# Optimization experiments

Measured on AMD Instinct MI355X. Metric: run time of the kernel, lower is better.

The kernel has to match this reference:

```python
import jax, jax.numpy as jnp
import numpy as np

N = 100000   # nodes
E = 1600000  # edges
IN = 128     # in_dim
H = 64       # hidden_dim
EPS = 1e-5


def layer_norm(x, g, b):
    mu = x.mean(-1, keepdims=True)
    v = ((x - mu) ** 2).mean(-1, keepdims=True)
    return (x - mu) * jax.lax.rsqrt(v + EPS) * g + b


def gcn_conv(x, W, b, src, dst, dinv):
    # PyG GCNConv: x' = D^{-1/2}(A+I)D^{-1/2} X W + b (degrees include self-loops)
    h = x @ W                                   # [N, H]
    coef = dinv[src] * dinv[dst]                # [E]
    agg = jax.ops.segment_sum(h[src] * coef[:, None], dst, num_segments=N)
    agg = agg + h * (dinv * dinv)[:, None]      # self-loop term
    return agg + b


def setup_inputs() -> dict:
    key = jax.random.key(0)
    ks = jax.random.split(key, 12)
    inp = {
        "x": jax.random.normal(ks[0], (N, IN), jnp.float32),
        "edge_index": jax.random.randint(ks[1], (2, E), 0, N, dtype=jnp.int64
                                         if jax.config.jax_enable_x64 else jnp.int32),
    }
    dims = [(IN, H), (H, H), (H, H)]
    for i, (di, do) in enumerate(dims, start=1):
        inp[f"W{i}"] = jax.random.normal(ks[2 * i], (di, do), jnp.float32) / np.sqrt(di)
        inp[f"b{i}"] = jnp.zeros((do,), jnp.float32)
        inp[f"g{i}"] = jnp.ones((do,), jnp.float32)
        inp[f"be{i}"] = jnp.zeros((do,), jnp.float32)
    inp["Wh"] = jax.random.normal(ks[11], (H, 1), jnp.float32) / np.sqrt(H)
    inp["bh"] = jnp.zeros((1,), jnp.float32)
    return inp


def reference(x, edge_index, W1, b1, g1, be1, W2, b2, g2, be2, W3, b3, g3, be3, Wh, bh):
    src, dst = edge_index[0], edge_index[1]
    deg = jax.ops.segment_sum(jnp.ones((E,), x.dtype), dst, num_segments=N) + 1.0
    dinv = jax.lax.rsqrt(deg)
    for W, b, g, be in ((W1, b1, g1, be1), (W2, b2, g2, be2), (W3, b3, g3, be3)):
        x = gcn_conv(x, W, b, src, dst, dinv)
        x = layer_norm(x, g, be)
        x = jax.nn.gelu(x, approximate=False)  # F.gelu default = exact erf
        # dropout omitted (eval mode / deterministic reference)
    return (x @ Wh + bh).squeeze(-1)  # [N]
```

## Files before the change

### kernel.cpp

```cpp
#include <hip/hip_runtime.h>
#include <math.h>

#define NODES 100000
#define EDGES 1600000
#define NBUCK 196
#define BCAP2 12288
#define EPB 4096
#define BINB 391
#define GEMMB 1563

typedef __attribute__((ext_vector_type(8))) short short8;
typedef __attribute__((ext_vector_type(4))) float floatx4;
typedef __attribute__((ext_vector_type(4))) unsigned uv4;

__device__ __forceinline__ float gsum8(float x) {
#pragma unroll
  for (int o = 4; o > 0; o >>= 1) x += __shfl_xor(x, o, 64);
  return x;
}

__device__ __forceinline__ short f2bf(float f) {
  union { float f; unsigned u; } v;
  v.f = f;
  unsigned r = 0x7fffu + ((v.u >> 16) & 1u);
  return (short)((v.u + r) >> 16);
}
__device__ __forceinline__ float bflo(unsigned p) {
  union { unsigned u; float f; } v; v.u = p << 16; return v.f;
}
__device__ __forceinline__ float bfhi(unsigned p) {
  union { unsigned u; float f; } v; v.u = p & 0xffff0000u; return v.f;
}

#define BIN_SMEM (4 * 256 * 4 + EPB * 4 + EPB)
__device__ __forceinline__ void bin_body(char* smemraw, int b, const int* __restrict__ src,
                                         const int* __restrict__ dst, int* __restrict__ bins,
                                         int* __restrict__ gcur) {
  int* cnt = (int*)smemraw;
  int* gb = cnt + 256;
  int* lb = gb + 256;
  int* lcur = lb + 256;
  int* rec = lcur + 256;
  unsigned char* rbk = (unsigned char*)(rec + EPB);
  int t = threadIdx.x;
  cnt[t] = 0;
  __syncthreads();
  int base = b * EPB;
  int nv = EDGES - base; if (nv > EPB) nv = EPB;
  int s[16], d[16];
#pragma unroll
  for (int j = 0; j < 16; ++j) {
    int e = base + j * 256 + t;
    if (e < EDGES) {
      s[j] = src[e];
      d[j] = dst[e];
      atomicAdd(&cnt[d[j] >> 9], 1);
    } else {
      d[j] = -1;
    }
  }
  __syncthreads();
  int c = cnt[t];
  lb[t] = c;
  __syncthreads();
  for (int o = 1; o < 256; o <<= 1) {
    int u = (t >= o) ? lb[t - o] : 0;
    __syncthreads();
    lb[t] += u;
    __syncthreads();
  }
  int ex = lb[t] - c;
  gb[t] = (c > 0) ? atomicAdd(&gcur[t], c) : 0;
  __syncthreads();
  lb[t] = ex;
  lcur[t] = ex;
  __syncthreads();
#pragma unroll
  for (int j = 0; j < 16; ++j) {
    if (d[j] >= 0) {
      int bk = d[j] >> 9;
      int lp = atomicAdd(&lcur[bk], 1);
      rec[lp] = s[j] | ((d[j] & 511) << 17);
      rbk[lp] = (unsigned char)bk;
    }
  }
  __syncthreads();
  for (int i = t; i < nv; i += 256) {
    int bk = rbk[i];
    int pos = gb[bk] + (i - lb[bk]);
    if (pos < BCAP2) bins[bk * BCAP2 + pos] = rec[i];
  }
}

#define FILL_SMEM (256 * 4 + 512 * 4 + 512 * 4 + 4 * 4 + BCAP2 * 4)
__device__ __forceinline__ void fill_body(char* smemraw, int b, const int* __restrict__ bins,
                                          const int* __restrict__ gcur, int* __restrict__ rowptr,
                                          float* __restrict__ dinv, int* __restrict__ csr) {
  int* bsm = (int*)smemraw;
  int* cnt = bsm + 256;
  int* cur = cnt + 512;
  int* wtot = cur + 512;
  int* stage = wtot + 4;
  int t = threadIdx.x;
  int v = 0;
  if (t < NBUCK) { v = gcur[t]; if (v > BCAP2) v = BCAP2; }
  bsm[t] = v;
  cnt[t] = 0; cnt[t + 256] = 0;
  __syncthreads();
  for (int o = 1; o < 256; o <<= 1) {
    int u = (t >= o) ? bsm[t - o] : 0;
    __syncthreads();
    bsm[t] += u;
    __syncthreads();
  }
  if (b == 0 && t == NBUCK - 1) rowptr[NODES] = bsm[t];
  int cb = gcur[b]; if (cb > BCAP2) cb = BCAP2;
  int bbase = bsm[b] - cb;
  const int* bp = &bins[(size_t)b * BCAP2];
  for (int i = t; i < cb; i += 256)
    atomicAdd(&cnt[(bp[i] >> 17) & 511], 1);
  __syncthreads();
  int a0 = cnt[2 * t], a1 = cnt[2 * t + 1];
  int sum2 = a0 + a1;
  int lane = t & 63, w = t >> 6;
  int inc = sum2;
#pragma unroll
  for (int o = 1; o < 64; o <<= 1) {
    int u = __shfl_up(inc, o, 64);
    if (lane >= o) inc += u;
  }
  if (lane == 63) wtot[w] = inc;
  __syncthreads();
  int wpre = 0;
  for (int ww = 0; ww < w; ++ww) wpre += wtot[ww];
  int l0 = wpre + inc - sum2;
  int l1 = l0 + a0;
  int n0 = b * 512 + 2 * t, n1 = n0 + 1;
  if (n0 < NODES) { rowptr[n0] = bbase + l0; dinv[n0] = rsqrtf((float)a0 + 1.0f); }
  if (n1 < NODES) { rowptr[n1] = bbase + l1; dinv[n1] = rsqrtf((float)a1 + 1.0f); }
  cur[2 * t] = l0; cur[2 * t + 1] = l1;
  __syncthreads();
  for (int i = t; i < cb; i += 256) {
    int pk = bp[i];
    int lp = atomicAdd(&cur[(pk >> 17) & 511], 1);
    stage[lp] = pk & 0x1FFFF;
  }
  __syncthreads();
  for (int i = t; i < cb; i += 256) csr[bbase + i] = stage[i];
}

#define GEMM_SMEM (64 * 136 * 2)
__device__ __forceinline__ void gemm_body(char* smemraw, int tile0, const float* __restrict__ x,
                                          const float* __restrict__ W, short* __restrict__ hs) {
  constexpr int K = 128, KP = K + 8;
  short* wt = (short*)smemraw;
  for (int idx = threadIdx.x; idx < K * 64; idx += 256) {
    int k = idx >> 6, n = idx & 63;
    wt[n * KP + k] = f2bf(W[idx]);
  }
  __syncthreads();
  int wid = threadIdx.x >> 6, lane = threadIdx.x & 63;
  int tile = tile0 + wid;
  if (tile * 16 >= NODES) return;
  int m = lane & 15, q = lane >> 4;

  short8 bfr[4][K / 32];
#pragma unroll
  for (int ct = 0; ct < 4; ++ct)
#pragma unroll
    for (int ks = 0; ks < K / 32; ++ks)
      bfr[ct][ks] = *reinterpret_cast<const short8*>(&wt[(ct * 16 + m) * KP + ks * 32 + q * 8]);

  floatx4 acc[4];
#pragma unroll
  for (int ct = 0; ct < 4; ++ct) acc[ct] = {0.f, 0.f, 0.f, 0.f};
  int r0 = tile * 16;
#pragma unroll
  for (int ks = 0; ks < K / 32; ++ks) {
    const float* xp = &x[(size_t)(r0 + m) * K + ks * 32 + q * 8];
    floatx4 a0 = *reinterpret_cast<const floatx4*>(xp);
    floatx4 a1 = *reinterpret_cast<const floatx4*>(xp + 4);
    short8 af;
#pragma unroll
    for (int j = 0; j < 4; ++j) { af[j] = f2bf(a0[j]); af[4 + j] = f2bf(a1[j]); }
#pragma unroll
    for (int ct = 0; ct < 4; ++ct)
      acc[ct] = __builtin_amdgcn_mfma_f32_16x16x32_bf16(af, bfr[ct][ks], acc[ct], 0, 0, 0);
  }
#pragma unroll
  for (int ct = 0; ct < 4; ++ct)
#pragma unroll
    for (int r = 0; r < 4; ++r) {
      int row = r0 + q * 4 + r, col = ct * 16 + m;
      hs[row * 64 + col] = f2bf(acc[ct][r]);
    }
}

__device__ __forceinline__ void prepw_body(int p, const float* __restrict__ W2,
                                           const float* __restrict__ W3,
                                           short* __restrict__ wt2, short* __restrict__ wt3) {
  const float* W = (p < 4) ? W2 : W3;
  short* wt = (p < 4) ? wt2 : wt3;
  int b0 = (p & 3) * 1024;
  for (int i = threadIdx.x; i < 1024; i += 256) {
    int e = b0 + i;
    int k = e >> 6, n = e & 63;
    wt[n * 72 + k] = f2bf(W[e]);
  }
}

template <bool PRESCALED>
__device__ __forceinline__ void do_agg(const uv4* __restrict__ hsv, const float* __restrict__ dinv,
                                       const int* __restrict__ csr, int n, int e0, int e1,
                                       int lane, float dn, float acc[8]) {
  int q = lane & 7, srcb = lane & 0x38;
  uv4 sv = hsv[(size_t)n * 8 + q];
#pragma unroll
  for (int w = 0; w < 4; ++w) {
    float lo = bflo(sv[w]), hi = bfhi(sv[w]);
    if constexpr (PRESCALED) { acc[2 * w] = lo; acc[2 * w + 1] = hi; }
    else { acc[2 * w] = lo * dn; acc[2 * w + 1] = hi * dn; }
  }
  for (int base = e0; base < e1; base += 8) {
    int cnt = e1 - base;
    if (cnt > 8) cnt = 8;
    int a = base + (q < cnt ? q : 0);
    int sidx = csr[a];
    float gq = 1.0f;
    if constexpr (!PRESCALED) gq = dinv[sidx];
    int s[8]; float wj[8];
#pragma unroll
    for (int j = 0; j < 8; ++j) {
      s[j] = __shfl(sidx, srcb | j, 64);
      if constexpr (!PRESCALED) {
        float bj = __shfl(gq, srcb | j, 64);
        wj[j] = (j < cnt) ? bj : 0.0f;
      } else {
        wj[j] = 1.0f;
      }
    }
    uv4 v[8];
#pragma unroll
    for (int j = 0; j < 8; ++j) v[j] = hsv[(size_t)s[j] * 8 + q];
    if constexpr (PRESCALED) {
      if (cnt == 8) {
#pragma unroll
        for (int j = 0; j < 8; ++j)
#pragma unroll
          for (int w = 0; w < 4; ++w) { acc[2 * w] += bflo(v[j][w]); acc[2 * w + 1] += bfhi(v[j][w]); }
      } else {
#pragma unroll
        for (int j = 0; j < 8; ++j)
          if (j < cnt)
#pragma unroll
            for (int w = 0; w < 4; ++w) { acc[2 * w] += bflo(v[j][w]); acc[2 * w + 1] += bfhi(v[j][w]); }
      }
    } else {
#pragma unroll
      for (int j = 0; j < 8; ++j)
#pragma unroll
        for (int w = 0; w < 4; ++w) {
          acc[2 * w]     += wj[j] * bflo(v[j][w]);
          acc[2 * w + 1] += wj[j] * bfhi(v[j][w]);
        }
    }
  }
}

template <bool PRESCALED>
__global__ __launch_bounds__(256) void k_aggg(const short* __restrict__ hs,
                                              const float* __restrict__ dinv,
                                              const int* __restrict__ rowptr,
                                              const int* __restrict__ csr,
                                              const float* __restrict__ bias,
                                              const float* __restrict__ gam,
                                              const float* __restrict__ bet,
                                              const short* __restrict__ wtg,
                                              short* __restrict__ hsn) {
  __shared__ __align__(16) short wt[64 * 72];
  __shared__ __align__(16) short ut[32 * 72];
  int t = threadIdx.x;
  {
    const int* wp = (const int*)wtg;
    int* wd = (int*)wt;
    for (int idx = t; idx < 2304; idx += 256) wd[idx] = wp[idx];
  }
  const uv4* hsv = (const uv4*)hs;
  int lane = t & 63, wid = t >> 6;
  int g = lane >> 3, q = lane & 7;
  int nb0 = blockIdx.x * 32;
  int r = wid * 8 + g;
  int n = nb0 + r;
  int e0 = rowptr[n], e1 = rowptr[n + 1];
  float dn = dinv[n];
  float acc[8];
  do_agg<PRESCALED>(hsv, dinv, csr, n, e0, e1, lane, dn, acc);

  const floatx4* bi4 = (const floatx4*)bias;
  floatx4 b0 = bi4[q * 2], b1 = bi4[q * 2 + 1];
#pragma unroll
  for (int f = 0; f < 4; ++f) { acc[f] = acc[f] * dn + b0[f]; acc[f + 4] = acc[f + 4] * dn + b1[f]; }

  float lsum = 0.f;
#pragma unroll
  for (int f = 0; f < 8; ++f) lsum += acc[f];
  float mu = gsum8(lsum) * (1.0f / 64.0f);
  float d[8], lvar = 0.f;
#pragma unroll
  for (int f = 0; f < 8; ++f) { d[f] = acc[f] - mu; lvar += d[f] * d[f]; }
  float rs = rsqrtf(gsum8(lvar) * (1.0f / 64.0f) + 1e-5f);
  const floatx4* gm4 = (const floatx4*)gam;
  const floatx4* bt4 = (const floatx4*)bet;
  floatx4 g0 = gm4[q * 2], g1 = gm4[q * 2 + 1];
  floatx4 t0 = bt4[q * 2], t1 = bt4[q * 2 + 1];
  short8 us;
#pragma unroll
  for (int f = 0; f < 8; ++f) {
    float gv = (f < 4) ? g0[f] : g1[f - 4];
    float tv = (f < 4) ? t0[f] : t1[f - 4];
    float vv = d[f] * rs * gv + tv;
    float u = 0.5f * vv * (1.0f + erff(vv * 0.70710678118654752f));
    us[f] = f2bf(u * dn);
  }
  *reinterpret_cast<short8*>(&ut[r * 72 + q * 8]) = us;
  __syncthreads();

  int m = lane & 15, q2 = lane >> 4;
  int tile = wid >> 1, cb = (wid & 1) * 2;
  short8 bfr[2][2];
#pragma unroll
  for (int ct = 0; ct < 2; ++ct)
#pragma unroll
    for (int ks = 0; ks < 2; ++ks)
      bfr[ct][ks] = *reinterpret_cast<const short8*>(&wt[((cb + ct) * 16 + m) * 72 + ks * 32 + q2 * 8]);
  floatx4 ac[2];
#pragma unroll
  for (int ct = 0; ct < 2; ++ct) ac[ct] = {0.f, 0.f, 0.f, 0.f};
#pragma unroll
  for (int ks = 0; ks < 2; ++ks) {
    short8 af = *reinterpret_cast<const short8*>(&ut[(tile * 16 + m) * 72 + ks * 32 + q2 * 8]);
#pragma unroll
    for (int ct = 0; ct < 2; ++ct)
      ac[ct] = __builtin_amdgcn_mfma_f32_16x16x32_bf16(af, bfr[ct][ks], ac[ct], 0, 0, 0);
  }
#pragma unroll
  for (int ct = 0; ct < 2; ++ct)
#pragma unroll
    for (int rr = 0; rr < 4; ++rr) {
      int row = nb0 + tile * 16 + q2 * 4 + rr, col = (cb + ct) * 16 + m;
      hsn[row * 64 + col] = f2bf(ac[ct][rr]);
    }
}

__global__ __launch_bounds__(256) void k_agg_fin(const short* __restrict__ hs,
                                                 const float* __restrict__ dinv,
                                                 const int* __restrict__ rowptr,
                                                 const int* __restrict__ csr,
                                                 const float* __restrict__ bias,
                                                 const float* __restrict__ gam,
                                                 const float* __restrict__ bet,
                                                 const float* __restrict__ Wh,
                                                 const float* __restrict__ bh,
                                                 float* __restrict__ out) {
  const uv4* hsv = (const uv4*)hs;
  int lane = threadIdx.x & 63, wid = threadIdx.x >> 6;
  int g = lane >> 3, q = lane & 7;
  int n = blockIdx.x * 32 + wid * 8 + g;
  int e0 = rowptr[n], e1 = rowptr[n + 1];
  float dn = dinv[n];
  float acc[8];
  do_agg<true>(hsv, dinv, csr, n, e0, e1, lane, dn, acc);
  const floatx4* bi4 = (const floatx4*)bias;
  floatx4 b0 = bi4[q * 2], b1 = bi4[q * 2 + 1];
#pragma unroll
  for (int f = 0; f < 4; ++f) { acc[f] = acc[f] * dn + b0[f]; acc[f + 4] = acc[f + 4] * dn + b1[f]; }
  float lsum = 0.f;
#pragma unroll
  for (int f = 0; f < 8; ++f) lsum += acc[f];
  float mu = gsum8(lsum) * (1.0f / 64.0f);
  float d[8], lvar = 0.f;
#pragma unroll
  for (int f = 0; f < 8; ++f) { d[f] = acc[f] - mu; lvar += d[f] * d[f]; }
  float rs = rsqrtf(gsum8(lvar) * (1.0f / 64.0f) + 1e-5f);
  const floatx4* gm4 = (const floatx4*)gam;
  const floatx4* bt4 = (const floatx4*)bet;
  floatx4 g0 = gm4[q * 2], g1 = gm4[q * 2 + 1];
  floatx4 t0 = bt4[q * 2], t1 = bt4[q * 2 + 1];
  const floatx4* wh4 = (const floatx4*)Wh;
  floatx4 w0 = wh4[q * 2], w1 = wh4[q * 2 + 1];
  float lp = 0.f;
#pragma unroll
  for (int f = 0; f < 8; ++f) {
    float gv = (f < 4) ? g0[f] : g1[f - 4];
    float tv = (f < 4) ? t0[f] : t1[f - 4];
    float wv = (f < 4) ? w0[f] : w1[f - 4];
    float vv = d[f] * rs * gv + tv;
    float u = 0.5f * vv * (1.0f + erff(vv * 0.70710678118654752f));
    lp += u * wv;
  }
  float p = gsum8(lp);
  if (q == 0) out[n] = p + bh[0];
}

__global__ __launch_bounds__(256) void k_pre1(const int* __restrict__ src, const int* __restrict__ dst,
                                              int* __restrict__ bins, int* __restrict__ gcur,
                                              const float* __restrict__ x, const float* __restrict__ W1,
                                              short* __restrict__ hs,
                                              const float* __restrict__ W2, const float* __restrict__ W3,
                                              short* __restrict__ wt2, short* __restrict__ wt3) {
  __shared__ __align__(16) char smem[BIN_SMEM];
  int b = blockIdx.x;
  if (b < BINB) bin_body(smem, b, src, dst, bins, gcur);
  else if (b < BINB + GEMMB) gemm_body(smem, (b - BINB) * 4, x, W1, hs);
  else prepw_body(b - BINB - GEMMB, W2, W3, wt2, wt3);
}

__global__ __launch_bounds__(256) void k_pre2(const int* __restrict__ bins, const int* __restrict__ gcur,
                                              int* __restrict__ rowptr, float* __restrict__ dinv,
                                              int* __restrict__ csr) {
  __shared__ __align__(16) char smem[FILL_SMEM];
  fill_body(smem, blockIdx.x, bins, gcur, rowptr, dinv, csr);
}

__global__ __launch_bounds__(256) void k_bin2(const int* src, const int* dst, int* bins, int* gcur) {
  __shared__ __align__(16) char smem[BIN_SMEM];
  bin_body(smem, blockIdx.x, src, dst, bins, gcur);
}
__global__ __launch_bounds__(256) void k_fillb2(const int* bins, const int* gcur, int* rowptr,
                                                float* dinv, int* csr) {
  __shared__ __align__(16) char smem[FILL_SMEM];
  fill_body(smem, blockIdx.x, bins, gcur, rowptr, dinv, csr);
}
__global__ __launch_bounds__(256) void k_gemm(const float* x, const float* W, short* hs) {
  __shared__ __align__(16) char smem[GEMM_SMEM];
  gemm_body(smem, blockIdx.x * 4, x, W, hs);
}
__global__ __launch_bounds__(256) void k_prepw(const float* W2, const float* W3, short* wt2, short* wt3) {
  prepw_body(blockIdx.x, W2, W3, wt2, wt3);
}

extern "C" void kernel_launch(void* const* d_in, const int* in_sizes, int n_in,
                              void* d_out, int out_size, void* d_ws, size_t ws_size,
                              hipStream_t stream) {
  const float* x  = (const float*)d_in[0];
  const int* ei   = (const int*)d_in[1];
  const float* W1 = (const float*)d_in[2];
  const float* b1 = (const float*)d_in[3];
  const float* g1 = (const float*)d_in[4];
  const float* be1= (const float*)d_in[5];
  const float* W2 = (const float*)d_in[6];
  const float* b2 = (const float*)d_in[7];
  const float* g2 = (const float*)d_in[8];
  const float* be2= (const float*)d_in[9];
  const float* W3 = (const float*)d_in[10];
  const float* b3 = (const float*)d_in[11];
  const float* g3 = (const float*)d_in[12];
  const float* be3= (const float*)d_in[13];
  const float* Wh = (const float*)d_in[14];
  const float* bh = (const float*)d_in[15];
  const int* srcp = ei;
  const int* dstp = ei + EDGES;

  char* ws = (char*)d_ws;
  size_t off = 0;
  auto take = [&](size_t bytes) {
    char* p = ws + off;
    off = (off + bytes + 255) & ~(size_t)255;
    return p;
  };
  float* dinv = (float*)take((size_t)NODES * 4);
  int* rowptr = (int*)take((size_t)(NODES + 1) * 4);
  int* csr    = (int*)take((size_t)EDGES * 4);
  short* hs_a = (short*)take((size_t)NODES * 64 * 2);
  short* hs_b = (short*)take((size_t)NODES * 64 * 2);
  short* wt2  = (short*)take((size_t)64 * 72 * 2);
  short* wt3  = (short*)take((size_t)64 * 72 * 2);

  size_t bins_sz = (size_t)NBUCK * BCAP2 * 4;
  bool overlap = (ws_size >= off + bins_sz + 4096);
  int* bins; int* gcur;
  if (overlap) {
    bins = (int*)take(bins_sz);
    gcur = (int*)take((size_t)NBUCK * 4);
  } else {
    bins = (int*)hs_a;
    gcur = (int*)hs_b;
  }

  (void)hipMemsetAsync(gcur, 0, (size_t)NBUCK * 4, stream);
  if (overlap) {
    k_pre1<<<BINB + GEMMB + 8, 256, 0, stream>>>(srcp, dstp, bins, gcur, x, W1, hs_a, W2, W3, wt2, wt3);
    k_pre2<<<NBUCK, 256, 0, stream>>>(bins, gcur, rowptr, dinv, csr);
  } else {
    k_bin2<<<BINB, 256, 0, stream>>>(srcp, dstp, bins, gcur);
    k_fillb2<<<NBUCK, 256, 0, stream>>>(bins, gcur, rowptr, dinv, csr);
    k_gemm<<<GEMMB, 256, 0, stream>>>(x, W1, hs_a);
    k_prepw<<<8, 256, 0, stream>>>(W2, W3, wt2, wt3);
  }
  k_aggg<false><<<NODES / 32, 256, 0, stream>>>(hs_a, dinv, rowptr, csr, b1, g1, be1, wt2, hs_b);
  k_aggg<true><<<NODES / 32, 256, 0, stream>>>(hs_b, dinv, rowptr, csr, b2, g2, be2, wt3, hs_a);
  k_agg_fin<<<NODES / 32, 256, 0, stream>>>(hs_a, dinv, rowptr, csr, b3, g3, be3, Wh, bh, (float*)d_out);
}
```

Measured before the change: 270.3 us.

## Prescale layer-1 features in fill pass and widen gather batches to 24 edges

The CSR fill kernel now multiplies the first-layer bf16 features by each node's dinv in place, so every aggregation layer can use the same prescaled gather path. That removes the per-edge dinv lookups and multiplies from layer 1. The gather loop now issues 24 neighbor loads per batch instead of 8, behind a scheduling barrier, to keep more memory requests in flight. Launch bounds are set to one block per SM minimum. The extra bf16 rounding of the prescaled features adds small numerical error, and the larger register footprint may lower occupancy.

```diff
diff --git a/kernel.cpp b/kernel.cpp
--- a/kernel.cpp
+++ b/kernel.cpp
@@ -30,6 +30,12 @@
 }
 __device__ __forceinline__ float bfhi(unsigned p) {
   union { unsigned u; float f; } v; v.u = p & 0xffff0000u; return v.f;
+}
+__device__ __forceinline__ unsigned scale2(unsigned p, float s) {
+  float lo = bflo(p) * s, hi = bfhi(p) * s;
+  unsigned ulo = (unsigned)(unsigned short)f2bf(lo);
+  unsigned uhi = (unsigned)(unsigned short)f2bf(hi);
+  return ulo | (uhi << 16);
 }
 
 #define BIN_SMEM (4 * 256 * 4 + EPB * 4 + EPB)
@@ -92,15 +98,17 @@
   }
 }
 
-#define FILL_SMEM (256 * 4 + 512 * 4 + 512 * 4 + 4 * 4 + BCAP2 * 4)
+#define FILL_SMEM (256 * 4 + 512 * 4 + 512 * 4 + 4 * 4 + BCAP2 * 4 + 512 * 4)
 __device__ __forceinline__ void fill_body(char* smemraw, int b, const int* __restrict__ bins,
                                           const int* __restrict__ gcur, int* __restrict__ rowptr,
-                                          float* __restrict__ dinv, int* __restrict__ csr) {
+                                          float* __restrict__ dinv, int* __restrict__ csr,
+                                          short* __restrict__ hs) {
   int* bsm = (int*)smemraw;
   int* cnt = bsm + 256;
   int* cur = cnt + 512;
   int* wtot = cur + 512;
   int* stage = wtot + 4;
+  float* dinvs = (float*)(stage + BCAP2);
   int t = threadIdx.x;
   int v = 0;
   if (t < NBUCK) { v = gcur[t]; if (v > BCAP2) v = BCAP2; }
@@ -136,8 +144,10 @@
   int l0 = wpre + inc - sum2;
   int l1 = l0 + a0;
   int n0 = b * 512 + 2 * t, n1 = n0 + 1;
-  if (n0 < NODES) { rowptr[n0] = bbase + l0; dinv[n0] = rsqrtf((float)a0 + 1.0f); }
-  if (n1 < NODES) { rowptr[n1] = bbase + l1; dinv[n1] = rsqrtf((float)a1 + 1.0f); }
+  float dv0 = rsqrtf((float)a0 + 1.0f), dv1 = rsqrtf((float)a1 + 1.0f);
+  if (n0 < NODES) { rowptr[n0] = bbase + l0; dinv[n0] = dv0; }
+  if (n1 < NODES) { rowptr[n1] = bbase + l1; dinv[n1] = dv1; }
+  dinvs[2 * t] = dv0; dinvs[2 * t + 1] = dv1;
   cur[2 * t] = l0; cur[2 * t + 1] = l1;
   __syncthreads();
   for (int i = t; i < cb; i += 256) {
@@ -147,6 +157,19 @@
   }
   __syncthreads();
   for (int i = t; i < cb; i += 256) csr[bbase + i] = stage[i];
+  uv4* hv = (uv4*)hs;
+  int nb = b * 512;
+  for (int i = t; i < 4096; i += 256) {
+    int row = i >> 3, ch = i & 7;
+    int n = nb + row;
+    if (n < NODES) {
+      float s = dinvs[row];
+      uv4 x = hv[(size_t)n * 8 + ch];
+#pragma unroll
+      for (int ww = 0; ww < 4; ++ww) x[ww] = scale2(x[ww], s);
+      hv[(size_t)n * 8 + ch] = x;
+    }
+  }
 }
 
 #define GEMM_SMEM (64 * 136 * 2)
@@ -209,74 +232,60 @@
   }
 }
 
-template <bool PRESCALED>
-__device__ __forceinline__ void do_agg(const uv4* __restrict__ hsv, const float* __restrict__ dinv,
-                                       const int* __restrict__ csr, int n, int e0, int e1,
-                                       int lane, float dn, float acc[8]) {
+__device__ __forceinline__ void do_agg24(const uv4* __restrict__ hsv, const int* __restrict__ csr,
+                                         int n, int e0, int e1, int lane, float acc[8]) {
   int q = lane & 7, srcb = lane & 0x38;
   uv4 sv = hsv[(size_t)n * 8 + q];
 #pragma unroll
-  for (int w = 0; w < 4; ++w) {
-    float lo = bflo(sv[w]), hi = bfhi(sv[w]);
-    if constexpr (PRESCALED) { acc[2 * w] = lo; acc[2 * w + 1] = hi; }
-    else { acc[2 * w] = lo * dn; acc[2 * w + 1] = hi * dn; }
-  }
-  for (int base = e0; base < e1; base += 8) {
-    int cnt = e1 - base;
-    if (cnt > 8) cnt = 8;
-    int a = base + (q < cnt ? q : 0);
-    int sidx = csr[a];
-    float gq = 1.0f;
-    if constexpr (!PRESCALED) gq = dinv[sidx];
-    int s[8]; float wj[8];
+  for (int w = 0; w < 4; ++w) { acc[2 * w] = bflo(sv[w]); acc[2 * w + 1] = bfhi(sv[w]); }
+  for (int base = e0; base < e1; base += 24) {
+    int rem = e1 - base;
+    int cnt = rem > 24 ? 24 : rem;
+    int p0 = base + q, p1 = p0 + 8, p2 = p0 + 16;
+    int i0 = csr[p0 < e1 ? p0 : e0];
+    int i1 = csr[p1 < e1 ? p1 : e0];
+    int i2 = csr[p2 < e1 ? p2 : e0];
+    uv4 v[24];
 #pragma unroll
     for (int j = 0; j < 8; ++j) {
-      s[j] = __shfl(sidx, srcb | j, 64);
-      if constexpr (!PRESCALED) {
-        float bj = __shfl(gq, srcb | j, 64);
-        wj[j] = (j < cnt) ? bj : 0.0f;
-      } else {
-        wj[j] = 1.0f;
-      }
-    }
-    uv4 v[8];
-#pragma unroll
-    for (int j = 0; j < 8; ++j) v[j] = hsv[(size_t)s[j] * 8 + q];
-    if constexpr (PRESCALED) {
-      if (cnt == 8) {
-#pragma unroll
-        for (int j = 0; j < 8; ++j)
+      int s = __shfl(i0, srcb | j, 64);
+      v[j] = hsv[(size_t)s * 8 + q];
+    }
+#pragma unroll
+    for (int j = 0; j < 8; ++j) {
+      int s = __shfl(i1, srcb | j, 64);
+      v[8 + j] = hsv[(size_t)s * 8 + q];
+    }
+#pragma unroll
+    for (int j = 0; j < 8; ++j) {
+      int s = __shfl(i2, srcb | j, 64);
+      v[16 + j] = hsv[(size_t)s * 8 + q];
+    }
+    __builtin_amdgcn_sched_barrier(0);
+    if (cnt == 24) {
+#pragma unroll
+      for (int j = 0; j < 24; ++j)
+#pragma unroll
+        for (int w = 0; w < 4; ++w) { acc[2 * w] += bflo(v[j][w]); acc[2 * w + 1] += bfhi(v[j][w]); }
+    } else {
+#pragma unroll
+      for (int j = 0; j < 24; ++j)
+        if (j < cnt)
 #pragma unroll
           for (int w = 0; w < 4; ++w) { acc[2 * w] += bflo(v[j][w]); acc[2 * w + 1] += bfhi(v[j][w]); }
-      } else {
-#pragma unroll
-        for (int j = 0; j < 8; ++j)
-          if (j < cnt)
-#pragma unroll
-            for (int w = 0; w < 4; ++w) { acc[2 * w] += bflo(v[j][w]); acc[2 * w + 1] += bfhi(v[j][w]); }
-      }
-    } else {
-#pragma unroll
-      for (int j = 0; j < 8; ++j)
-#pragma unroll
-        for (int w = 0; w < 4; ++w) {
-          acc[2 * w]     += wj[j] * bflo(v[j][w]);
-          acc[2 * w + 1] += wj[j] * bfhi(v[j][w]);
-        }
-    }
-  }
-}
-
-template <bool PRESCALED>
-__global__ __launch_bounds__(256) void k_aggg(const short* __restrict__ hs,
-                                              const float* __restrict__ dinv,
-                                              const int* __restrict__ rowptr,
-                                              const int* __restrict__ csr,
-                                              const float* __restrict__ bias,
-                                              const float* __restrict__ gam,
-                                              const float* __restrict__ bet,
-                                              const short* __restrict__ wtg,
-                                              short* __restrict__ hsn) {
+    }
+  }
+}
+
+__global__ __launch_bounds__(256, 1) void k_aggg(const short* __restrict__ hs,
+                                                 const float* __restrict__ dinv,
+                                                 const int* __restrict__ rowptr,
+                                                 const int* __restrict__ csr,
+                                                 const float* __restrict__ bias,
+                                                 const float* __restrict__ gam,
+                                                 const float* __restrict__ bet,
+                                                 const short* __restrict__ wtg,
+                                                 short* __restrict__ hsn) {
   __shared__ __align__(16) short wt[64 * 72];
   __shared__ __align__(16) short ut[32 * 72];
   int t = threadIdx.x;
@@ -294,7 +303,7 @@
   int e0 = rowptr[n], e1 = rowptr[n + 1];
   float dn = dinv[n];
   float acc[8];
-  do_agg<PRESCALED>(hsv, dinv, csr, n, e0, e1, lane, dn, acc);
+  do_agg24(hsv, csr, n, e0, e1, lane, acc);
 
   const floatx4* bi4 = (const floatx4*)bias;
   floatx4 b0 = bi4[q * 2], b1 = bi4[q * 2 + 1];
@@ -352,16 +361,16 @@
     }
 }
 
-__global__ __launch_bounds__(256) void k_agg_fin(const short* __restrict__ hs,
-                                                 const float* __restrict__ dinv,
-                                                 const int* __restrict__ rowptr,
-                                                 const int* __restrict__ csr,
-                                                 const float* __restrict__ bias,
-                                                 const float* __restrict__ gam,
-                                                 const float* __restrict__ bet,
-                                                 const float* __restrict__ Wh,
-                                                 const float* __restrict__ bh,
-                                                 float* __restrict__ out) {
+__global__ __launch_bounds__(256, 1) void k_agg_fin(const short* __restrict__ hs,
+                                                    const float* __restrict__ dinv,
+                                                    const int* __restrict__ rowptr,
+                                                    const int* __restrict__ csr,
+                                                    const float* __restrict__ bias,
+                                                    const float* __restrict__ gam,
+                                                    const float* __restrict__ bet,
+                                                    const float* __restrict__ Wh,
+                                                    const float* __restrict__ bh,
+                                                    float* __restrict__ out) {
   const uv4* hsv = (const uv4*)hs;
   int lane = threadIdx.x & 63, wid = threadIdx.x >> 6;
   int g = lane >> 3, q = lane & 7;
@@ -369,7 +378,7 @@
   int e0 = rowptr[n], e1 = rowptr[n + 1];
   float dn = dinv[n];
   float acc[8];
-  do_agg<true>(hsv, dinv, csr, n, e0, e1, lane, dn, acc);
+  do_agg24(hsv, csr, n, e0, e1, lane, acc);
   const floatx4* bi4 = (const floatx4*)bias;
   floatx4 b0 = bi4[q * 2], b1 = bi4[q * 2 + 1];
 #pragma unroll
@@ -417,9 +426,9 @@
 
 __global__ __launch_bounds__(256) void k_pre2(const int* __restrict__ bins, const int* __restrict__ gcur,
                                               int* __restrict__ rowptr, float* __restrict__ dinv,
-                                              int* __restrict__ csr) {
+                                              int* __restrict__ csr, short* __restrict__ hs) {
   __shared__ __align__(16) char smem[FILL_SMEM];
-  fill_body(smem, blockIdx.x, bins, gcur, rowptr, dinv, csr);
+  fill_body(smem, blockIdx.x, bins, gcur, rowptr, dinv, csr, hs);
 }
 
 __global__ __launch_bounds__(256) void k_bin2(const int* src, const int* dst, int* bins, int* gcur) {
@@ -427,9 +436,9 @@
   bin_body(smem, blockIdx.x, src, dst, bins, gcur);
 }
 __global__ __launch_bounds__(256) void k_fillb2(const int* bins, const int* gcur, int* rowptr,
-                                                float* dinv, int* csr) {
+                                                float* dinv, int* csr, short* hs) {
   __shared__ __align__(16) char smem[FILL_SMEM];
-  fill_body(smem, blockIdx.x, bins, gcur, rowptr, dinv, csr);
+  fill_body(smem, blockIdx.x, bins, gcur, rowptr, dinv, csr, hs);
 }
 __global__ __launch_bounds__(256) void k_gemm(const float* x, const float* W, short* hs) {
   __shared__ __align__(16) char smem[GEMM_SMEM];
@@ -490,14 +499,14 @@
   (void)hipMemsetAsync(gcur, 0, (size_t)NBUCK * 4, stream);
   if (overlap) {
     k_pre1<<<BINB + GEMMB + 8, 256, 0, stream>>>(srcp, dstp, bins, gcur, x, W1, hs_a, W2, W3, wt2, wt3);
-    k_pre2<<<NBUCK, 256, 0, stream>>>(bins, gcur, rowptr, dinv, csr);
+    k_pre2<<<NBUCK, 256, 0, stream>>>(bins, gcur, rowptr, dinv, csr, hs_a);
   } else {
     k_bin2<<<BINB, 256, 0, stream>>>(srcp, dstp, bins, gcur);
-    k_fillb2<<<NBUCK, 256, 0, stream>>>(bins, gcur, rowptr, dinv, csr);
     k_gemm<<<GEMMB, 256, 0, stream>>>(x, W1, hs_a);
     k_prepw<<<8, 256, 0, stream>>>(W2, W3, wt2, wt3);
-  }
-  k_aggg<false><<<NODES / 32, 256, 0, stream>>>(hs_a, dinv, rowptr, csr, b1, g1, be1, wt2, hs_b);
-  k_aggg<true><<<NODES / 32, 256, 0, stream>>>(hs_b, dinv, rowptr, csr, b2, g2, be2, wt3, hs_a);
+    k_fillb2<<<NBUCK, 256, 0, stream>>>(bins, gcur, rowptr, dinv, csr, hs_a);
+  }
+  k_aggg<<<NODES / 32, 256, 0, stream>>>(hs_a, dinv, rowptr, csr, b1, g1, be1, wt2, hs_b);
+  k_aggg<<<NODES / 32, 256, 0, stream>>>(hs_b, dinv, rowptr, csr, b2, g2, be2, wt3, hs_a);
   k_agg_fin<<<NODES / 32, 256, 0, stream>>>(hs_a, dinv, rowptr, csr, b3, g3, be3, Wh, bh, (float*)d_out);
 }
```

Result: slower. 281.5 us (+4.1%).
